# Kernel optimization log

Hardware: AMD Instinct MI355X
Metric: run time of the kernel (lower is better)

## Reference

```python
import jax, jax.numpy as jnp
import numpy as np

N_NODES = 100000
N_EDGES = 3200000
LATENT_DIM = 64


def _spmm(rows, cols, vals, x, num_segments):
    # y[i] = sum_{e: rows[e]==i} vals[e] * x[cols[e]]  -- COO sparse @ dense
    contrib = vals[:, None] * x[cols]          # [E, D]
    return jax.ops.segment_sum(contrib, rows, num_segments=num_segments)


def setup_inputs() -> dict:
    key = jax.random.key(0)
    k1, k2, k3, k4, k5 = jax.random.split(key, 5)
    x = jax.random.normal(k1, (N_NODES, LATENT_DIM), dtype=jnp.float32)
    alpha_train = jax.random.uniform(k2, (N_NODES,), dtype=jnp.float32)
    edge_rows = jax.random.randint(k3, (N_EDGES,), 0, N_NODES, dtype=jnp.int32)
    edge_cols = jax.random.randint(k4, (N_EDGES,), 0, N_NODES, dtype=jnp.int32)
    edge_vals = jax.random.uniform(k5, (N_EDGES,), dtype=jnp.float32)
    return {
        "t": 0,
        "x": x,
        "alpha_train": alpha_train,
        "edge_rows": edge_rows,
        "edge_cols": edge_cols,
        "edge_vals": edge_vals,
    }


def reference(t, x, alpha_train, edge_rows, edge_cols, edge_vals):
    # alph = sigmoid(alpha).unsqueeze(1)
    alph = jax.nn.sigmoid(alpha_train)[:, None]          # [N, 1]
    ax = _spmm(edge_rows, edge_cols, edge_vals, x, N_NODES)   # first hop: g @ x
    ax = alph * _spmm(edge_rows, edge_cols, edge_vals, ax, N_NODES)  # gated second hop
    f = ax - x                                           # residual
    return f
```

## Files before the change

kernel.cpp:

```cpp
#include <hip/hip_runtime.h>

#define LATENT 64
#define SUB_SHIFT 7
#define SUB_ROWS 128
#define COLBITS 17
#define COL_MASK ((1 << COLBITS) - 1)
#define HIST_BLOCKS 256
#define TILE 8192
#define NSUB_PAD 1024

__device__ __forceinline__ unsigned short f2bf(float f) {
    unsigned u = __float_as_uint(f);
    unsigned r = (u + 0x7FFFu + ((u >> 16) & 1u)) >> 16;
    return (unsigned short)r;
}

__global__ void subhist_kernel(const int* __restrict__ rows, int* __restrict__ part,
                               int E, int nsub) {
    __shared__ int h[NSUB_PAD];
    int t = threadIdx.x;
    for (int i = t; i < NSUB_PAD; i += blockDim.x) h[i] = 0;
    __syncthreads();
    for (int e = blockIdx.x * blockDim.x + t; e < E; e += gridDim.x * blockDim.x)
        atomicAdd(&h[rows[e] >> SUB_SHIFT], 1);
    __syncthreads();
    for (int i = t; i < nsub; i += blockDim.x) part[blockIdx.x * nsub + i] = h[i];
}

__global__ void reduce_partials_kernel(const int* __restrict__ part, int* __restrict__ tot,
                                       int nsub, int nblk) {
    __shared__ int s[256];
    int sidx = blockIdx.x;
    int t = threadIdx.x;
    int acc = 0;
    for (int b = t; b < nblk; b += 256) acc += part[b * nsub + sidx];
    s[t] = acc;
    __syncthreads();
    for (int o = 128; o > 0; o >>= 1) {
        if (t < o) s[t] += s[t + o];
        __syncthreads();
    }
    if (t == 0) tot[sidx] = s[0];
}

__global__ void subscan_kernel(const int* __restrict__ tot_in, int* __restrict__ csr0,
                               int* __restrict__ tstart, int* __restrict__ stot,
                               int* __restrict__ gcur, int nsub) {
    __shared__ int tot[NSUB_PAD];
    __shared__ int sc[256];
    int t = threadIdx.x;
    for (int i = t; i < NSUB_PAD; i += 256) tot[i] = (i < nsub) ? tot_in[i] : 0;
    __syncthreads();
    int c0 = tot[4 * t], c1 = tot[4 * t + 1], c2 = tot[4 * t + 2], c3 = tot[4 * t + 3];
    int csum = c0 + c1 + c2 + c3;
    sc[t] = csum;
    __syncthreads();
    for (int o = 1; o < 256; o <<= 1) {
        int u = (t >= o) ? sc[t - o] : 0;
        __syncthreads();
        sc[t] += u;
        __syncthreads();
    }
    int pre = sc[t] - csum;
    int s0 = 4 * t;
    if (s0 < nsub)     { csr0[s0] = pre;     stot[s0] = c0;     int ts = pre + 8 * s0;       tstart[s0] = ts;     gcur[s0] = ts; }
    pre += c0;
    if (s0 + 1 < nsub) { csr0[s0 + 1] = pre; stot[s0 + 1] = c1; int ts = pre + 8 * (s0 + 1); tstart[s0 + 1] = ts; gcur[s0 + 1] = ts; }
    pre += c1;
    if (s0 + 2 < nsub) { csr0[s0 + 2] = pre; stot[s0 + 2] = c2; int ts = pre + 8 * (s0 + 2); tstart[s0 + 2] = ts; gcur[s0 + 2] = ts; }
    pre += c2;
    if (s0 + 3 < nsub) { csr0[s0 + 3] = pre; stot[s0 + 3] = c3; int ts = pre + 8 * (s0 + 3); tstart[s0 + 3] = ts; gcur[s0 + 3] = ts; }
}

__global__ void conv_bf16_kernel(const float* __restrict__ in,
                                 unsigned short* __restrict__ outb, long long n4) {
    long long i = (long long)blockIdx.x * blockDim.x + threadIdx.x;
    long long stride = (long long)gridDim.x * blockDim.x;
    for (; i < n4; i += stride) {
        float4 f = reinterpret_cast<const float4*>(in)[i];
        ushort4 o;
        o.x = f2bf(f.x); o.y = f2bf(f.y); o.z = f2bf(f.z); o.w = f2bf(f.w);
        reinterpret_cast<ushort4*>(outb)[i] = o;
    }
}

__global__ void __launch_bounds__(512, 2) binscatter_kernel(
        const int* __restrict__ rows, const int* __restrict__ cols,
        const float* __restrict__ vals, int* __restrict__ gcur,
        int2* __restrict__ tmp, int E, int nsub) {
    __shared__ int hist[NSUB_PAD];
    __shared__ int base[NSUB_PAD];
    __shared__ int gbase[NSUB_PAD];
    __shared__ int2 stage[TILE];
    __shared__ int sc[512];
    int t = threadIdx.x;
    int tb = blockIdx.x * TILE;
    int tilecnt = E - tb; if (tilecnt > TILE) tilecnt = TILE;

    for (int i = t; i < NSUB_PAD; i += 512) hist[i] = 0;
    __syncthreads();
    #pragma unroll
    for (int k = 0; k < TILE / 512; ++k) {
        int e = tb + k * 512 + t;
        if (e < E) atomicAdd(&hist[rows[e] >> SUB_SHIFT], 1);
    }
    __syncthreads();
    int c0 = hist[2 * t], c1 = hist[2 * t + 1];
    int csum = c0 + c1;
    sc[t] = csum;
    __syncthreads();
    for (int o = 1; o < 512; o <<= 1) {
        int u = (t >= o) ? sc[t - o] : 0;
        __syncthreads();
        sc[t] += u;
        __syncthreads();
    }
    int ex = sc[t] - csum;
    base[2 * t] = ex;
    base[2 * t + 1] = ex + c0;
    __syncthreads();
    for (int i = t; i < NSUB_PAD; i += 512) hist[i] = 0;
    __syncthreads();
    #pragma unroll
    for (int k = 0; k < TILE / 512; ++k) {
        int e = tb + k * 512 + t;
        if (e < E) {
            int r = rows[e];
            int b = r >> SUB_SHIFT;
            int pos = base[b] + atomicAdd(&hist[b], 1);
            stage[pos] = make_int2(cols[e] | ((r & (SUB_ROWS - 1)) << COLBITS),
                                   __float_as_int(vals[e]));
        }
    }
    __syncthreads();
    for (int i = t; i < nsub; i += 512) {
        int n = hist[i];
        int gb = 0;
        if (n > 0) gb = atomicAdd(&gcur[i], n);
        gbase[i] = gb - base[i];
    }
    __syncthreads();
    for (int p = t; p < tilecnt; p += 512) {
        int lo = 0, hi = nsub;
        while (hi - lo > 1) { int mid = (lo + hi) >> 1; if (base[mid] <= p) lo = mid; else hi = mid; }
        tmp[gbase[lo] + p] = stage[p];
    }
}

__global__ void __launch_bounds__(512) subsort_kernel(
        const int2* __restrict__ tmp, const int* __restrict__ tstart,
        const int* __restrict__ stot, const int* __restrict__ csr0,
        int2* __restrict__ oc, int2* __restrict__ spair, int N) {
    __shared__ int lcnt[SUB_ROWS], lpos[SUB_ROWS], lcur[SUB_ROWS];
    int s = blockIdx.x;
    int t = threadIdx.x;
    int beg = tstart[s], n = stot[s], c0 = csr0[s];
    if (t < SUB_ROWS) lcnt[t] = 0;
    __syncthreads();
    for (int i = t; i < n; i += blockDim.x)
        atomicAdd(&lcnt[(tmp[beg + i].x >> COLBITS) & (SUB_ROWS - 1)], 1);
    __syncthreads();
    if (t < SUB_ROWS) lpos[t] = lcnt[t];
    __syncthreads();
    for (int o = 1; o < SUB_ROWS; o <<= 1) {
        int u = (t < SUB_ROWS && t >= o) ? lpos[t - o] : 0;
        __syncthreads();
        if (t < SUB_ROWS) lpos[t] += u;
        __syncthreads();
    }
    if (t < SUB_ROWS) {
        int excl = lpos[t] - lcnt[t];
        lcur[t] = excl;
        int row = (s << SUB_SHIFT) + t;
        if (row < N) oc[row] = make_int2(c0 + excl, lcnt[t]);
    }
    __syncthreads();
    for (int i = t; i < n; i += blockDim.x) {
        int2 w = tmp[beg + i];
        int rl = (w.x >> COLBITS) & (SUB_ROWS - 1);
        int p = atomicAdd(&lcur[rl], 1);
        spair[c0 + p] = make_int2(w.x & COL_MASK, w.y);
    }
}


#define FMA8(G, V)                                                              \
    acc0 += (V) * __uint_as_float((G).x << 16);                                 \
    acc1 += (V) * __uint_as_float((G).x & 0xFFFF0000u);                         \
    acc2 += (V) * __uint_as_float((G).y << 16);                                 \
    acc3 += (V) * __uint_as_float((G).y & 0xFFFF0000u);                         \
    acc4 += (V) * __uint_as_float((G).z << 16);                                 \
    acc5 += (V) * __uint_as_float((G).z & 0xFFFF0000u);                         \
    acc6 += (V) * __uint_as_float((G).w << 16);                                 \
    acc7 += (V) * __uint_as_float((G).w & 0xFFFF0000u);

#define GATHER_CORE(TBL)                                                        \
    int el = lane >> 3;                                                         \
    int f  = lane & 7;                                                          \
    const uint4* tb4 = (const uint4*)(TBL);                                     \
    const int2* sp = spair + el;                        \
    float acc0 = 0.f, acc1 = 0.f, acc2 = 0.f, acc3 = 0.f;                       \
    float acc4 = 0.f, acc5 = 0.f, acc6 = 0.f, acc7 = 0.f;                       \
    for (; e + 32 <= end; e += 32) {                                            \
        int2 w0 = sp[e];      int2 w1 = sp[e + 8];                              \
        int2 w2 = sp[e + 16]; int2 w3 = sp[e + 24];                             \
        uint4 g0 = tb4[(unsigned)w0.x * 8u + (unsigned)f];                      \
        uint4 g1 = tb4[(unsigned)w1.x * 8u + (unsigned)f];                      \
        uint4 g2 = tb4[(unsigned)w2.x * 8u + (unsigned)f];                      \
        uint4 g3 = tb4[(unsigned)w3.x * 8u + (unsigned)f];                      \
        float v0 = __int_as_float(w0.y), v1 = __int_as_float(w1.y);             \
        float v2 = __int_as_float(w2.y), v3 = __int_as_float(w3.y);             \
        FMA8(g0, v0)                                                            \
        FMA8(g1, v1)                                                            \
        FMA8(g2, v2)                                                            \
        FMA8(g3, v3)                                                            \
    }                                                                           \
    for (; e + 8 <= end; e += 8) {                                              \
        int2 w_ = sp[e];                                                        \
        uint4 g_ = tb4[(unsigned)w_.x * 8u + (unsigned)f];                      \
        float v_ = __int_as_float(w_.y);                                        \
        FMA8(g_, v_)                                                            \
    }                                                                           \
    if (e < end) {                                                              \
        int ei = e + el;                                                        \
        int ci = ei < end ? ei : end - 1;                                       \
        int2 w_ = spair[ci];                                                    \
        uint4 g_ = tb4[(unsigned)w_.x * 8u + (unsigned)f];                      \
        float v_ = (ei < end) ? __int_as_float(w_.y) : 0.f;                     \
        FMA8(g_, v_)                                                            \
    }                                                                           \
    acc0 += __shfl_xor(acc0, 8); acc0 += __shfl_xor(acc0, 16); acc0 += __shfl_xor(acc0, 32); \
    acc1 += __shfl_xor(acc1, 8); acc1 += __shfl_xor(acc1, 16); acc1 += __shfl_xor(acc1, 32); \
    acc2 += __shfl_xor(acc2, 8); acc2 += __shfl_xor(acc2, 16); acc2 += __shfl_xor(acc2, 32); \
    acc3 += __shfl_xor(acc3, 8); acc3 += __shfl_xor(acc3, 16); acc3 += __shfl_xor(acc3, 32); \
    acc4 += __shfl_xor(acc4, 8); acc4 += __shfl_xor(acc4, 16); acc4 += __shfl_xor(acc4, 32); \
    acc5 += __shfl_xor(acc5, 8); acc5 += __shfl_xor(acc5, 16); acc5 += __shfl_xor(acc5, 32); \
    acc6 += __shfl_xor(acc6, 8); acc6 += __shfl_xor(acc6, 16); acc6 += __shfl_xor(acc6, 32); \
    acc7 += __shfl_xor(acc7, 8); acc7 += __shfl_xor(acc7, 16); acc7 += __shfl_xor(acc7, 32);

__global__ void __launch_bounds__(256) spmm_gather1_kernel(
        const int2* __restrict__ oc, const int2* __restrict__ spair,
        const unsigned short* __restrict__ xb, unsigned short* __restrict__ axb, int N) {
    int wid = blockIdx.x * (blockDim.x >> 6) + (threadIdx.x >> 6);
    int lane = threadIdx.x & 63;
    if (wid >= N) return;
    int2 o = oc[wid];
    int e = o.x, end = o.x + o.y;
    GATHER_CORE(xb)
    if (el == 0) {
        uint4 pk;
        pk.x = (unsigned)f2bf(acc0) | ((unsigned)f2bf(acc1) << 16);
        pk.y = (unsigned)f2bf(acc2) | ((unsigned)f2bf(acc3) << 16);
        pk.z = (unsigned)f2bf(acc4) | ((unsigned)f2bf(acc5) << 16);
        pk.w = (unsigned)f2bf(acc6) | ((unsigned)f2bf(acc7) << 16);
        ((uint4*)axb)[(size_t)wid * 8 + f] = pk;
    }
}

__global__ void __launch_bounds__(256) spmm_gather2_kernel(
        const int2* __restrict__ oc, const int2* __restrict__ spair,
        const unsigned short* __restrict__ axb, const float* __restrict__ alpha,
        const float* __restrict__ x, float* __restrict__ out, int N) {
    int wid = blockIdx.x * (blockDim.x >> 6) + (threadIdx.x >> 6);
    int lane = threadIdx.x & 63;
    if (wid >= N) return;
    int2 o = oc[wid];
    int e = o.x, end = o.x + o.y;
    GATHER_CORE(axb)
    if (el == 0) {
        float a = 1.0f / (1.0f + __expf(-alpha[wid]));
        float4 xv0 = ((const float4*)x)[(size_t)wid * 16 + 2 * f];
        float4 xv1 = ((const float4*)x)[(size_t)wid * 16 + 2 * f + 1];
        float4 ov0, ov1;
        ov0.x = a * acc0 - xv0.x;
        ov0.y = a * acc1 - xv0.y;
        ov0.z = a * acc2 - xv0.z;
        ov0.w = a * acc3 - xv0.w;
        ov1.x = a * acc4 - xv1.x;
        ov1.y = a * acc5 - xv1.y;
        ov1.z = a * acc6 - xv1.z;
        ov1.w = a * acc7 - xv1.w;
        ((float4*)out)[(size_t)wid * 16 + 2 * f] = ov0;
        ((float4*)out)[(size_t)wid * 16 + 2 * f + 1] = ov1;
    }
}

__global__ void spmm_atomic_kernel(const int* __restrict__ rows, const int* __restrict__ cols,
                                   const float* __restrict__ vals, const float* __restrict__ x,
                                   float* __restrict__ y, int E) {
    long long tid = (long long)blockIdx.x * blockDim.x + threadIdx.x;
    long long total = (long long)E * 16;
    long long stride = (long long)gridDim.x * blockDim.x;
    for (; tid < total; tid += stride) {
        int e = (int)(tid >> 4);
        int q = (int)(tid & 15);
        int r = rows[e];
        int c = cols[e];
        float v = vals[e];
        float4 xv = reinterpret_cast<const float4*>(x)[(size_t)c * 16 + q];
        float* yp = y + (size_t)r * LATENT + q * 4;
        atomicAdd(yp + 0, v * xv.x);
        atomicAdd(yp + 1, v * xv.y);
        atomicAdd(yp + 2, v * xv.z);
        atomicAdd(yp + 3, v * xv.w);
    }
}

__global__ void finalize_kernel(const float* __restrict__ alpha, const float* __restrict__ x,
                                float* __restrict__ out, int N) {
    long long tid = (long long)blockIdx.x * blockDim.x + threadIdx.x;
    long long total = (long long)N * 16;
    long long stride = (long long)gridDim.x * blockDim.x;
    for (; tid < total; tid += stride) {
        int i = (int)(tid >> 4);
        float a = 1.0f / (1.0f + __expf(-alpha[i]));
        float4 ov = reinterpret_cast<float4*>(out)[tid];
        float4 xv = reinterpret_cast<const float4*>(x)[tid];
        ov.x = a * ov.x - xv.x;
        ov.y = a * ov.y - xv.y;
        ov.z = a * ov.z - xv.z;
        ov.w = a * ov.w - xv.w;
        reinterpret_cast<float4*>(out)[tid] = ov;
    }
}


extern "C" void kernel_launch(void* const* d_in, const int* in_sizes, int n_in,
                              void* d_out, int out_size, void* d_ws, size_t ws_size,
                              hipStream_t stream) {
    const float* x     = (const float*)d_in[1];
    const float* alpha = (const float*)d_in[2];
    const int*   rows  = (const int*)d_in[3];
    const int*   cols  = (const int*)d_in[4];
    const float* vals  = (const float*)d_in[5];

    const int N = in_sizes[2];
    const int E = in_sizes[3];
    float* out = (float*)d_out;

    const int block = 256;
    const int nsub   = (N + SUB_ROWS - 1) >> SUB_SHIFT;
    const int ntiles = (E + TILE - 1) / TILE;

    auto align256 = [](size_t v) { return (v + 255) & ~(size_t)255; };

    size_t tmp_bytes  = ((size_t)E + 8 * (size_t)nsub) * sizeof(int2);
    size_t xbf_bytes  = (size_t)N * LATENT * sizeof(unsigned short);
    size_t o_axbf_inA = align256(xbf_bytes);
    size_t bf_bytes   = o_axbf_inA + xbf_bytes;
    size_t RA = tmp_bytes > bf_bytes ? tmp_bytes : bf_bytes;

    size_t o_tmp    = 0;
    size_t o_spair  = align256(o_tmp + RA);
    size_t o_oc     = align256(o_spair + (size_t)E * sizeof(int2));
    size_t o_csr0   = align256(o_oc + (size_t)N * sizeof(int2));
    size_t o_tstart = align256(o_csr0 + (size_t)nsub * sizeof(int));
    size_t o_stot   = align256(o_tstart + (size_t)nsub * sizeof(int));
    size_t o_gcur   = align256(o_stot + (size_t)nsub * sizeof(int));
    size_t o_tot    = align256(o_gcur + (size_t)nsub * sizeof(int));
    size_t needed   = o_tot + (size_t)nsub * sizeof(int);
    size_t part_bytes = (size_t)HIST_BLOCKS * nsub * sizeof(int);

    if (ws_size >= needed && nsub <= NSUB_PAD && N <= (1 << COLBITS) &&
        part_bytes <= (size_t)E * sizeof(int2)) {
        char* ws = (char*)d_ws;
        int2*           tmp    = (int2*)(ws + o_tmp);
        unsigned short* xbf    = (unsigned short*)(ws + o_tmp);
        unsigned short* axbf   = (unsigned short*)(ws + o_tmp + o_axbf_inA);
        int2*           spair  = (int2*)(ws + o_spair);
        int*            part   = (int*)(ws + o_spair);
        int2*           oc     = (int2*)(ws + o_oc);
        int*            csr0   = (int*)(ws + o_csr0);
        int*            tstart = (int*)(ws + o_tstart);
        int*            stot   = (int*)(ws + o_stot);
        int*            gcur   = (int*)(ws + o_gcur);
        int*            tot    = (int*)(ws + o_tot);

        subhist_kernel<<<HIST_BLOCKS, 256, 0, stream>>>(rows, part, E, nsub);
        reduce_partials_kernel<<<nsub, 256, 0, stream>>>(part, tot, nsub, HIST_BLOCKS);
        subscan_kernel<<<1, 256, 0, stream>>>(tot, csr0, tstart, stot, gcur, nsub);

        binscatter_kernel<<<ntiles, 512, 0, stream>>>(rows, cols, vals, gcur, tmp, E, nsub);
        subsort_kernel<<<nsub, 512, 0, stream>>>(tmp, tstart, stot, csr0, oc, spair, N);

        long long n4 = (long long)N * (LATENT / 4);
        conv_bf16_kernel<<<2048, 256, 0, stream>>>(x, xbf, n4);

        int rows_per_block = block / 64;
        int grid_rows = (N + rows_per_block - 1) / rows_per_block;
        spmm_gather1_kernel<<<grid_rows, block, 0, stream>>>(oc, spair, xbf, axbf, N);
        spmm_gather2_kernel<<<grid_rows, block, 0, stream>>>(oc, spair, axbf,
                                                             alpha, x, out, N);
        return;
    }

    {
        float* ax1 = (float*)d_ws;
        const size_t feat_bytes = (size_t)N * LATENT * sizeof(float);
        hipMemsetAsync(ax1, 0, feat_bytes, stream);
        hipMemsetAsync(out, 0, feat_bytes, stream);
        long long work = (long long)E * 16;
        int grid_spmm = (int)((work + block - 1) / block);
        spmm_atomic_kernel<<<grid_spmm, block, 0, stream>>>(rows, cols, vals, x, ax1, E);
        spmm_atomic_kernel<<<grid_spmm, block, 0, stream>>>(rows, cols, vals, ax1, out, E);
        long long fwork = (long long)N * 16;
        int grid_fin = (int)((fwork + block - 1) / block);
        finalize_kernel<<<grid_fin, block, 0, stream>>>(alpha, x, out, N);
    }
}
```

Baseline: 209.8 us.

## Replace atomic bin-scatter with per-tile histogram prefix scan and direct placement

The radix-style bucketing of edges into row sub-blocks is restructured. Each tile now writes its own histogram, a per-bucket scan across tiles gives deterministic tile offsets, and a placement kernel scatters edges straight to their final global slots. This drops the global atomic cursor, the shared-memory staging buffer and the binary-search copy-out of the old binscatter kernel. In exchange, rows is read twice (once in the histogram pass, once in placement), global writes are less coalesced because they no longer go out in sorted order, and the tile size is halved so more partial histograms must be scanned.

```diff
diff --git a/kernel.cpp b/kernel.cpp
--- a/kernel.cpp
+++ b/kernel.cpp
@@ -5,8 +5,7 @@
 #define SUB_ROWS 128
 #define COLBITS 17
 #define COL_MASK ((1 << COLBITS) - 1)
-#define HIST_BLOCKS 256
-#define TILE 8192
+#define TILE 4096
 #define NSUB_PAD 1024
 
 __device__ __forceinline__ unsigned short f2bf(float f) {
@@ -15,37 +14,43 @@
     return (unsigned short)r;
 }
 
-__global__ void subhist_kernel(const int* __restrict__ rows, int* __restrict__ part,
-                               int E, int nsub) {
+__global__ void __launch_bounds__(512) hist_kernel(const int* __restrict__ rows,
+                                                   int* __restrict__ part, int E, int nsub) {
     __shared__ int h[NSUB_PAD];
     int t = threadIdx.x;
-    for (int i = t; i < NSUB_PAD; i += blockDim.x) h[i] = 0;
-    __syncthreads();
-    for (int e = blockIdx.x * blockDim.x + t; e < E; e += gridDim.x * blockDim.x)
-        atomicAdd(&h[rows[e] >> SUB_SHIFT], 1);
-    __syncthreads();
-    for (int i = t; i < nsub; i += blockDim.x) part[blockIdx.x * nsub + i] = h[i];
-}
-
-__global__ void reduce_partials_kernel(const int* __restrict__ part, int* __restrict__ tot,
-                                       int nsub, int nblk) {
-    __shared__ int s[256];
-    int sidx = blockIdx.x;
-    int t = threadIdx.x;
-    int acc = 0;
-    for (int b = t; b < nblk; b += 256) acc += part[b * nsub + sidx];
-    s[t] = acc;
-    __syncthreads();
-    for (int o = 128; o > 0; o >>= 1) {
-        if (t < o) s[t] += s[t + o];
-        __syncthreads();
-    }
-    if (t == 0) tot[sidx] = s[0];
+    int tb = blockIdx.x * TILE;
+    for (int i = t; i < NSUB_PAD; i += 512) h[i] = 0;
+    __syncthreads();
+    #pragma unroll
+    for (int k = 0; k < TILE / 512; ++k) {
+        int e = tb + k * 512 + t;
+        if (e < E) atomicAdd(&h[rows[e] >> SUB_SHIFT], 1);
+    }
+    __syncthreads();
+    for (int i = t; i < nsub; i += 512) part[blockIdx.x * nsub + i] = h[i];
+}
+
+__global__ void __launch_bounds__(1024) scanparts_kernel(int* __restrict__ part,
+                                                         int* __restrict__ tot,
+                                                         int nsub, int ntiles) {
+    __shared__ int sc[1024];
+    int s = blockIdx.x;
+    int t = threadIdx.x;
+    int v = (t < ntiles) ? part[t * nsub + s] : 0;
+    sc[t] = v;
+    __syncthreads();
+    for (int o = 1; o < 1024; o <<= 1) {
+        int u = (t >= o) ? sc[t - o] : 0;
+        __syncthreads();
+        sc[t] += u;
+        __syncthreads();
+    }
+    if (t < ntiles) part[t * nsub + s] = sc[t] - v;
+    if (t == 1023) tot[s] = sc[1023];
 }
 
 __global__ void subscan_kernel(const int* __restrict__ tot_in, int* __restrict__ csr0,
-                               int* __restrict__ tstart, int* __restrict__ stot,
-                               int* __restrict__ gcur, int nsub) {
+                               int* __restrict__ tstart, int* __restrict__ stot, int nsub) {
     __shared__ int tot[NSUB_PAD];
     __shared__ int sc[256];
     int t = threadIdx.x;
@@ -63,13 +68,38 @@
     }
     int pre = sc[t] - csum;
     int s0 = 4 * t;
-    if (s0 < nsub)     { csr0[s0] = pre;     stot[s0] = c0;     int ts = pre + 8 * s0;       tstart[s0] = ts;     gcur[s0] = ts; }
+    if (s0 < nsub)     { csr0[s0] = pre;     stot[s0] = c0;     tstart[s0] = pre + 8 * s0; }
     pre += c0;
-    if (s0 + 1 < nsub) { csr0[s0 + 1] = pre; stot[s0 + 1] = c1; int ts = pre + 8 * (s0 + 1); tstart[s0 + 1] = ts; gcur[s0 + 1] = ts; }
+    if (s0 + 1 < nsub) { csr0[s0 + 1] = pre; stot[s0 + 1] = c1; tstart[s0 + 1] = pre + 8 * (s0 + 1); }
     pre += c1;
-    if (s0 + 2 < nsub) { csr0[s0 + 2] = pre; stot[s0 + 2] = c2; int ts = pre + 8 * (s0 + 2); tstart[s0 + 2] = ts; gcur[s0 + 2] = ts; }
+    if (s0 + 2 < nsub) { csr0[s0 + 2] = pre; stot[s0 + 2] = c2; tstart[s0 + 2] = pre + 8 * (s0 + 2); }
     pre += c2;
-    if (s0 + 3 < nsub) { csr0[s0 + 3] = pre; stot[s0 + 3] = c3; int ts = pre + 8 * (s0 + 3); tstart[s0 + 3] = ts; gcur[s0 + 3] = ts; }
+    if (s0 + 3 < nsub) { csr0[s0 + 3] = pre; stot[s0 + 3] = c3; tstart[s0 + 3] = pre + 8 * (s0 + 3); }
+}
+
+__global__ void __launch_bounds__(512) place_kernel(
+        const int* __restrict__ rows, const int* __restrict__ cols,
+        const float* __restrict__ vals, const int* __restrict__ part,
+        const int* __restrict__ tstart, int2* __restrict__ tmp, int E, int nsub) {
+    __shared__ int gbase[NSUB_PAD];
+    __shared__ int cur[NSUB_PAD];
+    int t = threadIdx.x;
+    int tb = blockIdx.x * TILE;
+    for (int i = t; i < nsub; i += 512)
+        gbase[i] = part[blockIdx.x * nsub + i] + tstart[i];
+    for (int i = t; i < NSUB_PAD; i += 512) cur[i] = 0;
+    __syncthreads();
+    #pragma unroll
+    for (int k = 0; k < TILE / 512; ++k) {
+        int e = tb + k * 512 + t;
+        if (e < E) {
+            int r = rows[e];
+            int b = r >> SUB_SHIFT;
+            int p = gbase[b] + atomicAdd(&cur[b], 1);
+            tmp[p] = make_int2(cols[e] | ((r & (SUB_ROWS - 1)) << COLBITS),
+                               __float_as_int(vals[e]));
+        }
+    }
 }
 
 __global__ void conv_bf16_kernel(const float* __restrict__ in,
@@ -81,69 +111,6 @@
         ushort4 o;
         o.x = f2bf(f.x); o.y = f2bf(f.y); o.z = f2bf(f.z); o.w = f2bf(f.w);
         reinterpret_cast<ushort4*>(outb)[i] = o;
-    }
-}
-
-__global__ void __launch_bounds__(512, 2) binscatter_kernel(
-        const int* __restrict__ rows, const int* __restrict__ cols,
-        const float* __restrict__ vals, int* __restrict__ gcur,
-        int2* __restrict__ tmp, int E, int nsub) {
-    __shared__ int hist[NSUB_PAD];
-    __shared__ int base[NSUB_PAD];
-    __shared__ int gbase[NSUB_PAD];
-    __shared__ int2 stage[TILE];
-    __shared__ int sc[512];
-    int t = threadIdx.x;
-    int tb = blockIdx.x * TILE;
-    int tilecnt = E - tb; if (tilecnt > TILE) tilecnt = TILE;
-
-    for (int i = t; i < NSUB_PAD; i += 512) hist[i] = 0;
-    __syncthreads();
-    #pragma unroll
-    for (int k = 0; k < TILE / 512; ++k) {
-        int e = tb + k * 512 + t;
-        if (e < E) atomicAdd(&hist[rows[e] >> SUB_SHIFT], 1);
-    }
-    __syncthreads();
-    int c0 = hist[2 * t], c1 = hist[2 * t + 1];
-    int csum = c0 + c1;
-    sc[t] = csum;
-    __syncthreads();
-    for (int o = 1; o < 512; o <<= 1) {
-        int u = (t >= o) ? sc[t - o] : 0;
-        __syncthreads();
-        sc[t] += u;
-        __syncthreads();
-    }
-    int ex = sc[t] - csum;
-    base[2 * t] = ex;
-    base[2 * t + 1] = ex + c0;
-    __syncthreads();
-    for (int i = t; i < NSUB_PAD; i += 512) hist[i] = 0;
-    __syncthreads();
-    #pragma unroll
-    for (int k = 0; k < TILE / 512; ++k) {
-        int e = tb + k * 512 + t;
-        if (e < E) {
-            int r = rows[e];
-            int b = r >> SUB_SHIFT;
-            int pos = base[b] + atomicAdd(&hist[b], 1);
-            stage[pos] = make_int2(cols[e] | ((r & (SUB_ROWS - 1)) << COLBITS),
-                                   __float_as_int(vals[e]));
-        }
-    }
-    __syncthreads();
-    for (int i = t; i < nsub; i += 512) {
-        int n = hist[i];
-        int gb = 0;
-        if (n > 0) gb = atomicAdd(&gcur[i], n);
-        gbase[i] = gb - base[i];
-    }
-    __syncthreads();
-    for (int p = t; p < tilecnt; p += 512) {
-        int lo = 0, hi = nsub;
-        while (hi - lo > 1) { int mid = (lo + hi) >> 1; if (base[mid] <= p) lo = mid; else hi = mid; }
-        tmp[gbase[lo] + p] = stage[p];
     }
 }
 
@@ -356,13 +323,12 @@
     size_t o_csr0   = align256(o_oc + (size_t)N * sizeof(int2));
     size_t o_tstart = align256(o_csr0 + (size_t)nsub * sizeof(int));
     size_t o_stot   = align256(o_tstart + (size_t)nsub * sizeof(int));
-    size_t o_gcur   = align256(o_stot + (size_t)nsub * sizeof(int));
-    size_t o_tot    = align256(o_gcur + (size_t)nsub * sizeof(int));
+    size_t o_tot    = align256(o_stot + (size_t)nsub * sizeof(int));
     size_t needed   = o_tot + (size_t)nsub * sizeof(int);
-    size_t part_bytes = (size_t)HIST_BLOCKS * nsub * sizeof(int);
+    size_t part_bytes = (size_t)ntiles * nsub * sizeof(int);
 
     if (ws_size >= needed && nsub <= NSUB_PAD && N <= (1 << COLBITS) &&
-        part_bytes <= (size_t)E * sizeof(int2)) {
+        ntiles <= 1024 && part_bytes <= (size_t)E * sizeof(int2)) {
         char* ws = (char*)d_ws;
         int2*           tmp    = (int2*)(ws + o_tmp);
         unsigned short* xbf    = (unsigned short*)(ws + o_tmp);
@@ -373,14 +339,12 @@
         int*            csr0   = (int*)(ws + o_csr0);
         int*            tstart = (int*)(ws + o_tstart);
         int*            stot   = (int*)(ws + o_stot);
-        int*            gcur   = (int*)(ws + o_gcur);
         int*            tot    = (int*)(ws + o_tot);
 
-        subhist_kernel<<<HIST_BLOCKS, 256, 0, stream>>>(rows, part, E, nsub);
-        reduce_partials_kernel<<<nsub, 256, 0, stream>>>(part, tot, nsub, HIST_BLOCKS);
-        subscan_kernel<<<1, 256, 0, stream>>>(tot, csr0, tstart, stot, gcur, nsub);
-
-        binscatter_kernel<<<ntiles, 512, 0, stream>>>(rows, cols, vals, gcur, tmp, E, nsub);
+        hist_kernel<<<ntiles, 512, 0, stream>>>(rows, part, E, nsub);
+        scanparts_kernel<<<nsub, 1024, 0, stream>>>(part, tot, nsub, ntiles);
+        subscan_kernel<<<1, 256, 0, stream>>>(tot, csr0, tstart, stot, nsub);
+        place_kernel<<<ntiles, 512, 0, stream>>>(rows, cols, vals, part, tstart, tmp, E, nsub);
         subsort_kernel<<<nsub, 512, 0, stream>>>(tmp, tstart, stot, csr0, oc, spair, N);
 
         long long n4 = (long long)N * (LATENT / 4);
```

Measured after the change: 215.2 us. 1.03x slower.
